# Optimization experiments

Hardware: AMD Instinct MI355X
Metric: run time of the kernel (lower is better)

The kernel has to match this reference:

```python
import jax, jax.numpy as jnp
import numpy as np

N_NODES = 200000  # num_users + num_items
N_EDGES = 500000
LATENT = 64
N_LAYERS = 3
NEG_SLOPE = 0.01  # F.leaky_relu default
EPS = 1e-16       # PyG geo_softmax denominator epsilon


def setup_inputs() -> dict:
    key = jax.random.key(0)
    k1, k2, k3, k4, k5 = jax.random.split(key, 5)
    edge_index = jax.random.randint(k1, (2, N_EDGES), 0, N_NODES, dtype=jnp.int64 if jax.config.jax_enable_x64 else jnp.int32)
    edge_attrs = jax.random.normal(k2, (N_EDGES, 2), dtype=jnp.float32)
    emb = jax.random.normal(k3, (N_NODES, LATENT), dtype=jnp.float32)
    # per-layer attention params, shape [L, heads=1 -> squeezed, in_channels]
    a_att_w = jax.random.normal(k4, (N_LAYERS, LATENT), dtype=jnp.float32) * 0.1
    r_att_w = jax.random.normal(k5, (N_LAYERS, LATENT), dtype=jnp.float32) * 0.1
    return {"edge_index": edge_index, "edge_attrs": edge_attrs, "emb": emb,
            "a_att_w": a_att_w, "r_att_w": r_att_w}


def _segment_softmax(scores, dst, num_nodes):
    # scores: [E, D] softmax over edges grouped by destination node (PyG geo_softmax)
    m = jax.ops.segment_max(scores, dst, num_segments=num_nodes)  # [N, D]
    m = jnp.where(jnp.isfinite(m), m, 0.0)  # nodes without incoming edges
    w = jnp.exp(scores - m[dst])
    den = jax.ops.segment_sum(w, dst, num_segments=num_nodes)     # [N, D]
    return w / (den[dst] + EPS)


def reference(edge_index, edge_attrs, emb, a_att_w, r_att_w):
    src, dst = edge_index[0], edge_index[1]
    n = emb.shape[0]
    # symmetric degree normalization (degree of destination endpoints)
    deg = jax.ops.segment_sum(jnp.ones_like(dst, dtype=emb.dtype), dst, num_segments=n)
    dinv = jnp.where(deg > 0, deg ** -0.5, 0.0)
    norm = (dinv[src] * dinv[dst])[:, None]  # [E, 1]

    a_e = edge_attrs[:, 0:1]  # [E, 1]
    r_e = edge_attrs[:, 1:2]

    x = emb
    acc = emb  # layer-0 embedding
    for l in range(N_LAYERS):
        scores = (jax.nn.leaky_relu(a_e * a_att_w[l], NEG_SLOPE)
                  + jax.nn.leaky_relu(r_e * r_att_w[l], NEG_SLOPE))  # [E, D]
        attn = _segment_softmax(scores, dst, n)                       # [E, D]
        msg = norm * attn * x[src]                                    # gather + weight
        x = jax.ops.segment_sum(msg, dst, num_segments=n)             # scatter-add
        acc = acc + x
    out = acc / (N_LAYERS + 1)  # mean over layer embeddings
    return out
```

## Files before the change

kernel.cpp:

```cpp
#include <hip/hip_runtime.h>

#define BLK 256
#define LBLK 1024


__global__ void k_deg(const int* __restrict__ dst, int* __restrict__ deg, int E) {
    int e = blockIdx.x * blockDim.x + threadIdx.x;
    if (e < E) atomicAdd(&deg[dst[e]], 1);
}

__global__ void k_scan1(const int* __restrict__ deg, int* __restrict__ partials,
                        int N, int chunk) {
    __shared__ int sm[BLK];
    int b = blockIdx.x;
    int start = b * chunk;
    int end = min(start + chunk, N);
    int s = 0;
    for (int i = start + threadIdx.x; i < end; i += BLK) s += deg[i];
    sm[threadIdx.x] = s;
    __syncthreads();
    for (int off = BLK / 2; off > 0; off >>= 1) {
        if (threadIdx.x < off) sm[threadIdx.x] += sm[threadIdx.x + off];
        __syncthreads();
    }
    if (threadIdx.x == 0) partials[b] = sm[0];
}

__global__ void k_scan2(int* __restrict__ partials, int* __restrict__ row_off,
                        int N, int E) {
    __shared__ int sm[BLK];
    int t = threadIdx.x;
    sm[t] = partials[t];
    __syncthreads();
    for (int off = 1; off < BLK; off <<= 1) {
        int add = (t >= off) ? sm[t - off] : 0;
        __syncthreads();
        sm[t] += add;
        __syncthreads();
    }
    partials[t] = (t == 0) ? 0 : sm[t - 1];
    if (t == 0) row_off[N] = E;
}

__global__ void k_scan3(const int* __restrict__ deg, const int* __restrict__ partials,
                        int* __restrict__ row_off, int* __restrict__ cursor,
                        int N, int chunk) {
    __shared__ int sm[BLK];
    int b = blockIdx.x;
    int base = partials[b];
    int start = b * chunk;
    int end = min(start + chunk, N);
    for (int tile = start; tile < end; tile += BLK) {
        int idx = tile + threadIdx.x;
        int val = (idx < end) ? deg[idx] : 0;
        sm[threadIdx.x] = val;
        __syncthreads();
        for (int off = 1; off < BLK; off <<= 1) {
            int add = (threadIdx.x >= off) ? sm[threadIdx.x - off] : 0;
            __syncthreads();
            sm[threadIdx.x] += add;
            __syncthreads();
        }
        int excl = sm[threadIdx.x] - val;
        if (idx < end) {
            row_off[idx] = base + excl;
            cursor[idx]  = base + excl;
        }
        int tile_total = sm[BLK - 1];
        __syncthreads();
        base += tile_total;
    }
}

__global__ void k_fill(const int* __restrict__ src, const int* __restrict__ dst,
                       const float* __restrict__ attrs, const int* __restrict__ deg,
                       int* __restrict__ cursor, float4* __restrict__ csr, int E) {
    int e = blockIdx.x * blockDim.x + threadIdx.x;
    if (e >= E) return;
    int s = src[e], t = dst[e];
    int pos = atomicAdd(&cursor[t], 1);
    float a = attrs[2 * e];
    float r = attrs[2 * e + 1];
    int ds = deg[s], dt = deg[t];
    float nrm = (ds > 0) ? (1.0f / sqrtf((float)ds * (float)dt)) : 0.0f;
    csr[pos] = make_float4(__int_as_float(s), a, r, nrm);
}


__device__ __forceinline__ float lrelu(float x) { return x > 0.0f ? x : 0.01f * x; }

__device__ __forceinline__ float4 edge_w4(float a, float r, const float4& aw, const float4& rw) {
    float4 w;
    w.x = __expf(lrelu(a * aw.x) + lrelu(r * rw.x));
    w.y = __expf(lrelu(a * aw.y) + lrelu(r * rw.y));
    w.z = __expf(lrelu(a * aw.z) + lrelu(r * rw.z));
    w.w = __expf(lrelu(a * aw.w) + lrelu(r * rw.w));
    return w;
}

__device__ __forceinline__ void acc4(float4& num, float4& den, float nrm,
                                     const float4& w, const float4& xv) {
    den.x += w.x; den.y += w.y; den.z += w.z; den.w += w.w;
    num.x += nrm * w.x * xv.x;
    num.y += nrm * w.y * xv.y;
    num.z += nrm * w.z * xv.z;
    num.w += nrm * w.w * xv.w;
}

template<int MODE>
__global__ __launch_bounds__(LBLK) void k_layer(
    const float4* __restrict__ x4, const float4* __restrict__ csr,
    const int* __restrict__ row_off,
    const float4* __restrict__ aw4, const float4* __restrict__ rw4,
    const float4* __restrict__ emb4, const float4* __restrict__ xA4,
    const float4* __restrict__ xB4,
    float4* __restrict__ xout4, float4* __restrict__ out4, int N) {
    const int t = threadIdx.x;
    const int d4 = t & 15;
    const int nl = t >> 4;
    const int v = blockIdx.x * (LBLK / 16) + nl;
    if (v >= N) return;
    const float4 aw = aw4[d4];
    const float4 rw = rw4[d4];
    const int s0 = row_off[v];
    const int s1 = row_off[v + 1];
    float4 num = {0.f, 0.f, 0.f, 0.f};
    float4 den = {0.f, 0.f, 0.f, 0.f};
    for (int i = s0; i < s1; i += 2) {
        const int last = s1 - 1;
        float4 e0 = csr[i];
        float4 e1 = csr[min(i + 1, last)];
        float4 x0 = x4[(size_t)(unsigned)__float_as_int(e0.x) * 16 + d4];
        float4 x1 = x4[(size_t)(unsigned)__float_as_int(e1.x) * 16 + d4];
        float4 w0 = edge_w4(e0.y, e0.z, aw, rw);
        float4 w1 = edge_w4(e1.y, e1.z, aw, rw);
        float g1 = (i + 1 < s1) ? 1.0f : 0.0f;
        w1.x *= g1; w1.y *= g1; w1.z *= g1; w1.w *= g1;
        acc4(num, den, e0.w, w0, x0);
        acc4(num, den, e1.w, w1, x1);
    }
    float4 xn;
    xn.x = num.x / (den.x + 1e-16f);
    xn.y = num.y / (den.y + 1e-16f);
    xn.z = num.z / (den.z + 1e-16f);
    xn.w = num.w / (den.w + 1e-16f);
    const size_t o = (size_t)v * 16 + d4;
    if (MODE == 2) {
        float4 e = emb4[o], A = xA4[o], B = xB4[o];
        float4 r;
        r.x = (e.x + A.x + B.x + xn.x) * 0.25f;
        r.y = (e.y + A.y + B.y + xn.y) * 0.25f;
        r.z = (e.z + A.z + B.z + xn.z) * 0.25f;
        r.w = (e.w + A.w + B.w + xn.w) * 0.25f;
        out4[o] = r;
    } else {
        xout4[o] = xn;
    }
}


extern "C" void kernel_launch(void* const* d_in, const int* in_sizes, int n_in,
                              void* d_out, int out_size, void* d_ws, size_t ws_size,
                              hipStream_t stream) {
    const int*   ei    = (const int*)d_in[0];
    const float* attrs = (const float*)d_in[1];
    const float* emb   = (const float*)d_in[2];
    const float* a_att = (const float*)d_in[3];
    const float* r_att = (const float*)d_in[4];

    const int E = in_sizes[0] / 2;
    const int N = in_sizes[2] / 64;
    const int* src = ei;
    const int* dst = ei + E;

    char* ws = (char*)d_ws;
    size_t off = 0;
    auto alloc = [&](size_t bytes) {
        void* p = ws + off;
        off += (bytes + 255) & ~(size_t)255;
        return p;
    };
    int*    deg      = (int*)alloc((size_t)N * 4);
    int*    row_off  = (int*)alloc((size_t)(N + 1) * 4);
    int*    cursor   = (int*)alloc((size_t)N * 4);
    int*    partials = (int*)alloc((size_t)BLK * 4);
    float4* csr      = (float4*)alloc((size_t)E * 16);
    float4* xA       = (float4*)alloc((size_t)N * 64 * 4);
    float4* xB       = (float4*)alloc((size_t)N * 64 * 4);
    float4* out      = (float4*)d_out;

    hipMemsetAsync(deg, 0, (size_t)N * 4, stream);

    int gE = (E + BLK - 1) / BLK;
    int chunk = (N + BLK - 1) / BLK;

    k_deg  <<<gE, BLK, 0, stream>>>(dst, deg, E);
    k_scan1<<<BLK, BLK, 0, stream>>>(deg, partials, N, chunk);
    k_scan2<<<1,   BLK, 0, stream>>>(partials, row_off, N, E);
    k_scan3<<<BLK, BLK, 0, stream>>>(deg, partials, row_off, cursor, N, chunk);
    k_fill <<<gE, BLK, 0, stream>>>(src, dst, attrs, deg, cursor, csr, E);

    const float4* emb4 = (const float4*)emb;
    const float4* aw4  = (const float4*)a_att;
    const float4* rw4  = (const float4*)r_att;

    int gL = (N + (LBLK / 16) - 1) / (LBLK / 16);
    k_layer<0><<<gL, LBLK, 0, stream>>>(emb4, csr, row_off, aw4,      rw4,
                                        nullptr, nullptr, nullptr, xA, nullptr, N);
    k_layer<1><<<gL, LBLK, 0, stream>>>(xA,   csr, row_off, aw4 + 16, rw4 + 16,
                                        nullptr, nullptr, nullptr, xB, nullptr, N);
    k_layer<2><<<gL, LBLK, 0, stream>>>(xB,   csr, row_off, aw4 + 32, rw4 + 32,
                                        emb4, xA, xB, nullptr, out, N);
}
```

Measured before the change: 295.4 us.

## Store layer embeddings in bf16 with folded degree scaling and atomic-free CSR fill

Intermediate layer features are stored as bf16, pre-scaled by dinv of the source node, so the per-edge norm multiply drops out of the gather loop and gather traffic is halved. The CSR fill now uses ranks recorded during the degree atomics, which removes the second atomic pass. The two scan kernels are merged into one, the layer block size is reduced, and a conversion kernel produces the scaled bf16 embeddings. The cost is bf16 rounding error in the gathered features and one extra conversion pass.

```diff
diff --git a/kernel.cpp b/kernel.cpp
--- a/kernel.cpp
+++ b/kernel.cpp
@@ -1,12 +1,29 @@
 #include <hip/hip_runtime.h>
 
 #define BLK 256
-#define LBLK 1024
-
-
-__global__ void k_deg(const int* __restrict__ dst, int* __restrict__ deg, int E) {
+#define LBLK 256
+
+__device__ __forceinline__ unsigned short f2bf(float f) {
+    unsigned u = __float_as_uint(f);
+    u += 0x7FFFu + ((u >> 16) & 1u);
+    return (unsigned short)(u >> 16);
+}
+__device__ __forceinline__ float bf2f(unsigned short h) {
+    return __uint_as_float((unsigned)h << 16);
+}
+__device__ __forceinline__ float4 unpack4(ushort4 h) {
+    return make_float4(bf2f(h.x), bf2f(h.y), bf2f(h.z), bf2f(h.w));
+}
+__device__ __forceinline__ ushort4 pack4(float4 f) {
+    ushort4 h; h.x = f2bf(f.x); h.y = f2bf(f.y); h.z = f2bf(f.z); h.w = f2bf(f.w);
+    return h;
+}
+
+
+__global__ void k_deg(const int* __restrict__ dst, int* __restrict__ deg,
+                      int* __restrict__ rank, int E) {
     int e = blockIdx.x * blockDim.x + threadIdx.x;
-    if (e < E) atomicAdd(&deg[dst[e]], 1);
+    if (e < E) rank[e] = atomicAdd(&deg[dst[e]], 1);
 }
 
 __global__ void k_scan1(const int* __restrict__ deg, int* __restrict__ partials,
@@ -26,64 +43,62 @@
     if (threadIdx.x == 0) partials[b] = sm[0];
 }
 
-__global__ void k_scan2(int* __restrict__ partials, int* __restrict__ row_off,
-                        int N, int E) {
+__global__ void k_scan23(const int* __restrict__ deg, const int* __restrict__ partials,
+                         int* __restrict__ row_off, int N, int E, int chunk) {
+    __shared__ int sp[BLK];
     __shared__ int sm[BLK];
+    int b = blockIdx.x;
     int t = threadIdx.x;
-    sm[t] = partials[t];
+    sp[t] = partials[t];
     __syncthreads();
     for (int off = 1; off < BLK; off <<= 1) {
-        int add = (t >= off) ? sm[t - off] : 0;
-        __syncthreads();
-        sm[t] += add;
-        __syncthreads();
-    }
-    partials[t] = (t == 0) ? 0 : sm[t - 1];
-    if (t == 0) row_off[N] = E;
-}
-
-__global__ void k_scan3(const int* __restrict__ deg, const int* __restrict__ partials,
-                        int* __restrict__ row_off, int* __restrict__ cursor,
-                        int N, int chunk) {
-    __shared__ int sm[BLK];
-    int b = blockIdx.x;
-    int base = partials[b];
+        int add = (t >= off) ? sp[t - off] : 0;
+        __syncthreads();
+        sp[t] += add;
+        __syncthreads();
+    }
+    int base = (b == 0) ? 0 : sp[b - 1];
+    if (b == 0 && t == 0) row_off[N] = E;
+    __syncthreads();
     int start = b * chunk;
     int end = min(start + chunk, N);
     for (int tile = start; tile < end; tile += BLK) {
-        int idx = tile + threadIdx.x;
+        int idx = tile + t;
         int val = (idx < end) ? deg[idx] : 0;
-        sm[threadIdx.x] = val;
+        sm[t] = val;
         __syncthreads();
         for (int off = 1; off < BLK; off <<= 1) {
-            int add = (threadIdx.x >= off) ? sm[threadIdx.x - off] : 0;
+            int add = (t >= off) ? sm[t - off] : 0;
             __syncthreads();
-            sm[threadIdx.x] += add;
+            sm[t] += add;
             __syncthreads();
         }
-        int excl = sm[threadIdx.x] - val;
-        if (idx < end) {
-            row_off[idx] = base + excl;
-            cursor[idx]  = base + excl;
-        }
+        if (idx < end) row_off[idx] = base + sm[t] - val;
         int tile_total = sm[BLK - 1];
         __syncthreads();
         base += tile_total;
     }
 }
 
+__global__ void k_conv(const float4* __restrict__ emb4, const int* __restrict__ deg,
+                       ushort4* __restrict__ embs, int N16) {
+    int i = blockIdx.x * blockDim.x + threadIdx.x;
+    if (i >= N16) return;
+    int v = i >> 4;
+    int d = deg[v];
+    float dinv = (d > 0) ? rsqrtf((float)d) : 0.0f;
+    float4 e = emb4[i];
+    embs[i] = pack4(make_float4(dinv * e.x, dinv * e.y, dinv * e.z, dinv * e.w));
+}
+
 __global__ void k_fill(const int* __restrict__ src, const int* __restrict__ dst,
-                       const float* __restrict__ attrs, const int* __restrict__ deg,
-                       int* __restrict__ cursor, float4* __restrict__ csr, int E) {
+                       const float* __restrict__ attrs, const int* __restrict__ row_off,
+                       const int* __restrict__ rank, float4* __restrict__ csr, int E) {
     int e = blockIdx.x * blockDim.x + threadIdx.x;
     if (e >= E) return;
-    int s = src[e], t = dst[e];
-    int pos = atomicAdd(&cursor[t], 1);
-    float a = attrs[2 * e];
-    float r = attrs[2 * e + 1];
-    int ds = deg[s], dt = deg[t];
-    float nrm = (ds > 0) ? (1.0f / sqrtf((float)ds * (float)dt)) : 0.0f;
-    csr[pos] = make_float4(__int_as_float(s), a, r, nrm);
+    int pos = row_off[dst[e]] + rank[e];
+    float2 ar = ((const float2*)attrs)[e];
+    csr[pos] = make_float4(__int_as_float(src[e]), ar.x, ar.y, 0.0f);
 }
 
 
@@ -98,63 +113,65 @@
     return w;
 }
 
-__device__ __forceinline__ void acc4(float4& num, float4& den, float nrm,
-                                     const float4& w, const float4& xv) {
-    den.x += w.x; den.y += w.y; den.z += w.z; den.w += w.w;
-    num.x += nrm * w.x * xv.x;
-    num.y += nrm * w.y * xv.y;
-    num.z += nrm * w.z * xv.z;
-    num.w += nrm * w.w * xv.w;
-}
-
 template<int MODE>
 __global__ __launch_bounds__(LBLK) void k_layer(
-    const float4* __restrict__ x4, const float4* __restrict__ csr,
-    const int* __restrict__ row_off,
+    const ushort4* __restrict__ xs, const float4* __restrict__ csr,
+    const int* __restrict__ row_off, const int* __restrict__ deg,
     const float4* __restrict__ aw4, const float4* __restrict__ rw4,
-    const float4* __restrict__ emb4, const float4* __restrict__ xA4,
-    const float4* __restrict__ xB4,
-    float4* __restrict__ xout4, float4* __restrict__ out4, int N) {
+    const float4* __restrict__ emb4,
+    const ushort4* __restrict__ xsA, const ushort4* __restrict__ xsB,
+    ushort4* __restrict__ xsout, float4* __restrict__ out4, int N) {
     const int t = threadIdx.x;
     const int d4 = t & 15;
-    const int nl = t >> 4;
-    const int v = blockIdx.x * (LBLK / 16) + nl;
+    const int v = blockIdx.x * (LBLK / 16) + (t >> 4);
     if (v >= N) return;
     const float4 aw = aw4[d4];
     const float4 rw = rw4[d4];
     const int s0 = row_off[v];
     const int s1 = row_off[v + 1];
+    const int dv = deg[v];
     float4 num = {0.f, 0.f, 0.f, 0.f};
     float4 den = {0.f, 0.f, 0.f, 0.f};
     for (int i = s0; i < s1; i += 2) {
         const int last = s1 - 1;
         float4 e0 = csr[i];
         float4 e1 = csr[min(i + 1, last)];
-        float4 x0 = x4[(size_t)(unsigned)__float_as_int(e0.x) * 16 + d4];
-        float4 x1 = x4[(size_t)(unsigned)__float_as_int(e1.x) * 16 + d4];
+        ushort4 h0 = xs[(size_t)(unsigned)__float_as_int(e0.x) * 16 + d4];
+        ushort4 h1 = xs[(size_t)(unsigned)__float_as_int(e1.x) * 16 + d4];
         float4 w0 = edge_w4(e0.y, e0.z, aw, rw);
         float4 w1 = edge_w4(e1.y, e1.z, aw, rw);
         float g1 = (i + 1 < s1) ? 1.0f : 0.0f;
         w1.x *= g1; w1.y *= g1; w1.z *= g1; w1.w *= g1;
-        acc4(num, den, e0.w, w0, x0);
-        acc4(num, den, e1.w, w1, x1);
-    }
-    float4 xn;
-    xn.x = num.x / (den.x + 1e-16f);
-    xn.y = num.y / (den.y + 1e-16f);
-    xn.z = num.z / (den.z + 1e-16f);
-    xn.w = num.w / (den.w + 1e-16f);
+        float4 x0 = unpack4(h0);
+        float4 x1 = unpack4(h1);
+        den.x += w0.x + w1.x; den.y += w0.y + w1.y;
+        den.z += w0.z + w1.z; den.w += w0.w + w1.w;
+        num.x += w0.x * x0.x + w1.x * x1.x;
+        num.y += w0.y * x0.y + w1.y * x1.y;
+        num.z += w0.z * x0.z + w1.z * x1.z;
+        num.w += w0.w * x0.w + w1.w * x1.w;
+    }
+    float4 xr;
+    xr.x = num.x / (den.x + 1e-16f);
+    xr.y = num.y / (den.y + 1e-16f);
+    xr.z = num.z / (den.z + 1e-16f);
+    xr.w = num.w / (den.w + 1e-16f);
+    const float dinv = (dv > 0) ? rsqrtf((float)dv) : 0.0f;
     const size_t o = (size_t)v * 16 + d4;
     if (MODE == 2) {
-        float4 e = emb4[o], A = xA4[o], B = xB4[o];
+        const float sd = (dv > 0) ? sqrtf((float)dv) : 0.0f;
+        float4 e = emb4[o];
+        float4 A = unpack4(xsA[o]);
+        float4 B = unpack4(xsB[o]);
         float4 r;
-        r.x = (e.x + A.x + B.x + xn.x) * 0.25f;
-        r.y = (e.y + A.y + B.y + xn.y) * 0.25f;
-        r.z = (e.z + A.z + B.z + xn.z) * 0.25f;
-        r.w = (e.w + A.w + B.w + xn.w) * 0.25f;
+        r.x = (e.x + sd * (A.x + B.x) + dinv * xr.x) * 0.25f;
+        r.y = (e.y + sd * (A.y + B.y) + dinv * xr.y) * 0.25f;
+        r.z = (e.z + sd * (A.z + B.z) + dinv * xr.z) * 0.25f;
+        r.w = (e.w + sd * (A.w + B.w) + dinv * xr.w) * 0.25f;
         out4[o] = r;
     } else {
-        xout4[o] = xn;
+        const float s = dinv * dinv;
+        xsout[o] = pack4(make_float4(s * xr.x, s * xr.y, s * xr.z, s * xr.w));
     }
 }
 
@@ -180,35 +197,36 @@
         off += (bytes + 255) & ~(size_t)255;
         return p;
     };
-    int*    deg      = (int*)alloc((size_t)N * 4);
-    int*    row_off  = (int*)alloc((size_t)(N + 1) * 4);
-    int*    cursor   = (int*)alloc((size_t)N * 4);
-    int*    partials = (int*)alloc((size_t)BLK * 4);
-    float4* csr      = (float4*)alloc((size_t)E * 16);
-    float4* xA       = (float4*)alloc((size_t)N * 64 * 4);
-    float4* xB       = (float4*)alloc((size_t)N * 64 * 4);
-    float4* out      = (float4*)d_out;
+    int*     deg      = (int*)alloc((size_t)N * 4);
+    int*     rank     = (int*)alloc((size_t)E * 4);
+    int*     row_off  = (int*)alloc((size_t)(N + 1) * 4);
+    int*     partials = (int*)alloc((size_t)BLK * 4);
+    float4*  csr      = (float4*)alloc((size_t)E * 16);
+    ushort4* embs     = (ushort4*)alloc((size_t)N * 16 * 8);
+    ushort4* xsA      = (ushort4*)alloc((size_t)N * 16 * 8);
+    ushort4* xsB      = (ushort4*)alloc((size_t)N * 16 * 8);
+    float4*  out      = (float4*)d_out;
 
     hipMemsetAsync(deg, 0, (size_t)N * 4, stream);
 
     int gE = (E + BLK - 1) / BLK;
     int chunk = (N + BLK - 1) / BLK;
 
-    k_deg  <<<gE, BLK, 0, stream>>>(dst, deg, E);
-    k_scan1<<<BLK, BLK, 0, stream>>>(deg, partials, N, chunk);
-    k_scan2<<<1,   BLK, 0, stream>>>(partials, row_off, N, E);
-    k_scan3<<<BLK, BLK, 0, stream>>>(deg, partials, row_off, cursor, N, chunk);
-    k_fill <<<gE, BLK, 0, stream>>>(src, dst, attrs, deg, cursor, csr, E);
+    k_deg   <<<gE, BLK, 0, stream>>>(dst, deg, rank, E);
+    k_scan1 <<<BLK, BLK, 0, stream>>>(deg, partials, N, chunk);
+    k_scan23<<<BLK, BLK, 0, stream>>>(deg, partials, row_off, N, E, chunk);
+    k_conv  <<<(N * 16 + BLK - 1) / BLK, BLK, 0, stream>>>((const float4*)emb, deg, embs, N * 16);
+    k_fill  <<<gE, BLK, 0, stream>>>(src, dst, attrs, row_off, rank, csr, E);
 
     const float4* emb4 = (const float4*)emb;
     const float4* aw4  = (const float4*)a_att;
     const float4* rw4  = (const float4*)r_att;
 
     int gL = (N + (LBLK / 16) - 1) / (LBLK / 16);
-    k_layer<0><<<gL, LBLK, 0, stream>>>(emb4, csr, row_off, aw4,      rw4,
-                                        nullptr, nullptr, nullptr, xA, nullptr, N);
-    k_layer<1><<<gL, LBLK, 0, stream>>>(xA,   csr, row_off, aw4 + 16, rw4 + 16,
-                                        nullptr, nullptr, nullptr, xB, nullptr, N);
-    k_layer<2><<<gL, LBLK, 0, stream>>>(xB,   csr, row_off, aw4 + 32, rw4 + 32,
-                                        emb4, xA, xB, nullptr, out, N);
-}
+    k_layer<0><<<gL, LBLK, 0, stream>>>(embs, csr, row_off, deg, aw4,      rw4,
+                                        nullptr, nullptr, nullptr, xsA, nullptr, N);
+    k_layer<1><<<gL, LBLK, 0, stream>>>(xsA,  csr, row_off, deg, aw4 + 16, rw4 + 16,
+                                        nullptr, nullptr, nullptr, xsB, nullptr, N);
+    k_layer<2><<<gL, LBLK, 0, stream>>>(xsB,  csr, row_off, deg, aw4 + 32, rw4 + 32,
+                                        emb4, xsA, xsB, nullptr, out, N);
+}
```

Result: faster. 257.1 us (-13.0%).
